# Optimization experiments

Measured on AMD Instinct MI355X. Metric: run time of the kernel, lower is better.

The kernel has to match this reference:

```python
import jax, jax.numpy as jnp
import numpy as np

B, S, D, H = 2, 2048, 1024, 16
HD = D // H


def setup_inputs() -> dict:
    key = jax.random.key(0)
    ks = jax.random.split(key, 5)
    x = jax.random.normal(ks[0], (B, S, D), dtype=jnp.float32)
    qk_w = jax.random.normal(ks[1], (D, 2 * D), dtype=jnp.float32) * 0.02
    qk_b = jnp.zeros((2 * D,), dtype=jnp.float32)
    v_w = jax.random.normal(ks[2], (D, D), dtype=jnp.float32) * 0.02
    cproj_w = jax.random.normal(ks[3], (D, D), dtype=jnp.float32) * 0.02
    resid_gain = jnp.ones((1, H, 1, 1), dtype=jnp.float32)
    skip_gain = jnp.ones((1, H, 1, 1), dtype=jnp.float32)
    centre_gain = jnp.ones((1, H, 1, 1), dtype=jnp.float32)
    return {"x": x, "qk_w": qk_w, "qk_b": qk_b, "v_w": v_w,
            "cproj_w": cproj_w, "resid_gain": resid_gain,
            "skip_gain": skip_gain, "centre_gain": centre_gain}


def reference(x, qk_w, qk_b, v_w, cproj_w, resid_gain, skip_gain, centre_gain):
    b, s, d = x.shape
    h, hd = H, d // H
    # fused QK projection (pconv with bias)
    qk = x @ qk_w + qk_b                      # [B,S,2D]
    q, k = jnp.split(qk, 2, axis=-1)
    v = x @ v_w                               # [B,S,D] (pconv, bias=0)
    # split heads -> [B,H,S,hd]
    q = q.reshape(b, s, h, hd).transpose(0, 2, 1, 3)
    k = k.reshape(b, s, h, hd).transpose(0, 2, 1, 3)
    v = v.reshape(b, s, h, hd).transpose(0, 2, 1, 3)
    # scaled QK^T with causal mask
    scores = jnp.einsum('bhqd,bhkd->bhqk', q, k) / jnp.sqrt(jnp.float32(hd))
    causal = jnp.tril(jnp.ones((s, s), dtype=bool))
    neg = jnp.finfo(scores.dtype).min
    scores = jnp.where(causal, scores, neg)
    attn = jax.nn.softmax(scores, axis=-1)    # [B,H,S,S]
    # shaped attention: per-head resid gain + skip (identity) - centred uniform causal
    row = jnp.arange(1, s + 1, dtype=jnp.float32)
    uniform = jnp.tril(jnp.ones((s, s), dtype=jnp.float32) / row[:, None])  # [S,S]
    eye = jnp.eye(s, dtype=jnp.float32)
    new_attn = (resid_gain * attn
                + skip_gain * eye[None, None]
                - centre_gain * uniform[None, None])
    out = jnp.einsum('bhqk,bhkd->bhqd', new_attn, v)  # [B,H,S,hd]
    out = out.transpose(0, 2, 1, 3).reshape(b, s, d)  # merge heads
    out = out @ cproj_w                                # c_proj (bias=0)
    return out
```

## Files before the change

### kernel.cpp

```cpp
#include <hip/hip_runtime.h>
#include <hip/hip_bf16.h>


typedef __hip_bfloat16 bf16;
typedef short s16x8 __attribute__((ext_vector_type(8)));
typedef short s16x4 __attribute__((ext_vector_type(4)));
typedef float f32x4 __attribute__((ext_vector_type(4)));

#define NB 2
#define NS 2048
#define ND 1024
#define NH 16
#define NHD 64
#define QSCALE 0.18033688011112042f
#define SW(r) (((r) & 7) << 4)

__device__ __forceinline__ float b2f(unsigned short u) {
  union { float f; unsigned int i; } c; c.i = ((unsigned int)u) << 16; return c.f;
}

__device__ __forceinline__ unsigned short f2bu(float f) {
  bf16 t = __float2bfloat16(f);
  unsigned short u;
  __builtin_memcpy(&u, &t, 2);
  return u;
}

__device__ __forceinline__ void gload_lds16(const void* g, void* l) {
  __builtin_amdgcn_global_load_lds((const __attribute__((address_space(1))) void*)g,
                                   (__attribute__((address_space(3))) void*)l, 16, 0, 0);
}

__global__ __launch_bounds__(256) void prologue(const float* __restrict__ x,
                                                const float* __restrict__ qk_w,
                                                const float* __restrict__ v_w,
                                                const float* __restrict__ cp_w,
                                                bf16* __restrict__ xb,
                                                bf16* __restrict__ qkwt,
                                                bf16* __restrict__ vwt,
                                                bf16* __restrict__ cpwt) {
  const int z = blockIdx.z;
  const int tx = threadIdx.x, ty = threadIdx.y;
  if (z == 0) {
    const int lb = (int)blockIdx.x + 64 * (int)blockIdx.y;
    const int base = lb * 2048 + (ty * 32 + tx) * 8;
    float4 v0 = *(const float4*)(x + base);
    float4 v1 = *(const float4*)(x + base + 4);
    ushort4 o0, o1;
    o0.x = f2bu(v0.x); o0.y = f2bu(v0.y); o0.z = f2bu(v0.z); o0.w = f2bu(v0.w);
    o1.x = f2bu(v1.x); o1.y = f2bu(v1.y); o1.z = f2bu(v1.z); o1.w = f2bu(v1.w);
    *(ushort4*)(xb + base) = o0;
    *(ushort4*)(xb + base + 4) = o1;
    return;
  }
  const int N = (z == 1) ? 2048 : 1024;
  if ((int)blockIdx.x * 32 >= N) return;
  const float* in = (z == 1) ? qk_w : (z == 2) ? v_w : cp_w;
  bf16* out = (z == 1) ? qkwt : (z == 2) ? vwt : cpwt;
  const int K = 1024;
  __shared__ float tile[32][33];
  int nt = blockIdx.x * 32, kt = blockIdx.y * 32;
#pragma unroll
  for (int j = 0; j < 32; j += 8)
    tile[ty + j][tx] = in[(size_t)(kt + ty + j) * N + nt + tx];
  __syncthreads();
#pragma unroll
  for (int j = 0; j < 32; j += 8)
    out[(size_t)(nt + ty + j) * K + kt + tx] = __float2bfloat16(tile[tx][ty + j]);
}

__global__ __launch_bounds__(256) void gemm_qkv(const bf16* __restrict__ A,
                                                const bf16* __restrict__ BtQK,
                                                const bf16* __restrict__ BtV,
                                                const float* __restrict__ bias,
                                                bf16* __restrict__ qo, bf16* __restrict__ ko,
                                                bf16* __restrict__ vo) {
  __shared__ alignas(16) bf16 As[128 * 32];
  __shared__ alignas(16) bf16 Bs[128 * 32];
  const int K = 1024;
  const int tid = threadIdx.x;
  const int wave = tid >> 6, lane = tid & 63;
  const int l15 = lane & 15, lg = lane >> 4;
  const int wr = wave >> 1, wc = wave & 1;
  const int bid = (int)blockIdx.x + (int)blockIdx.y * 24;
  const int sbid = (bid & 7) * 96 + (bid >> 3);
  const int brow = (sbid / 24) * 128, bcol = (sbid % 24) * 128;
  const bf16* Bsrc = (bcol < 2048) ? (BtQK + (size_t)bcol * K)
                                   : (BtV + (size_t)(bcol - 2048) * K);

  f32x4 acc[4][4] = {};
  const int r0 = tid >> 2;
  const int kc = (tid & 3) * 8;
  char* AsB = (char*)As;
  char* BsB = (char*)Bs;

  for (int k0 = 0; k0 < K; k0 += 32) {
    gload_lds16(A + (size_t)(brow + r0) * K + k0 + kc, AsB + tid * 16);
    gload_lds16(A + (size_t)(brow + r0 + 64) * K + k0 + kc, AsB + 4096 + tid * 16);
    gload_lds16(Bsrc + (size_t)r0 * K + k0 + kc, BsB + tid * 16);
    gload_lds16(Bsrc + (size_t)(r0 + 64) * K + k0 + kc, BsB + 4096 + tid * 16);
    __syncthreads();
    s16x8 af[4], bfr[4];
#pragma unroll
    for (int mi = 0; mi < 4; ++mi)
      af[mi] = *(const s16x8*)(As + (wr * 64 + mi * 16 + l15) * 32 + lg * 8);
#pragma unroll
    for (int ni = 0; ni < 4; ++ni)
      bfr[ni] = *(const s16x8*)(Bs + (wc * 64 + ni * 16 + l15) * 32 + lg * 8);
#pragma unroll
    for (int mi = 0; mi < 4; ++mi)
#pragma unroll
      for (int ni = 0; ni < 4; ++ni)
        acc[mi][ni] = __builtin_amdgcn_mfma_f32_16x16x32_bf16(af[mi], bfr[ni], acc[mi][ni], 0, 0, 0);
    __syncthreads();
  }

#pragma unroll
  for (int mi = 0; mi < 4; ++mi)
#pragma unroll
    for (int ni = 0; ni < 4; ++ni)
#pragma unroll
      for (int r = 0; r < 4; ++r) {
        int row = brow + wr * 64 + mi * 16 + lg * 4 + r;
        int col = bcol + wc * 64 + ni * 16 + l15;
        float v = acc[mi][ni][r];
        int b = row >> 11, s = row & 2047;
        int cc = col & 1023;
        int h = cc >> 6, e = cc & 63;
        if (col < 1024) {
          v = (v + bias[col]) * QSCALE;
          qo[((((size_t)b * NH + h) * NS) + s) * NHD + e] = __float2bfloat16(v);
        } else if (col < 2048) {
          v += bias[col];
          ko[((((size_t)b * NH + h) * NS) + s) * NHD + e] = __float2bfloat16(v);
        } else {
          vo[((((size_t)b * NH + h) * NHD) + e) * NS + s] = __float2bfloat16(v);
        }
      }
}

__global__ __launch_bounds__(256) void gemm_out(const bf16* __restrict__ A,
                                                const bf16* __restrict__ Bt,
                                                float* __restrict__ of) {
  __shared__ alignas(16) bf16 As[128 * 32];
  __shared__ alignas(16) bf16 Bs[64 * 32];
  const int K = 1024, N = 1024;
  const int tid = threadIdx.x;
  const int wave = tid >> 6, lane = tid & 63;
  const int l15 = lane & 15, lg = lane >> 4;
  const int bid = (int)blockIdx.x + (int)blockIdx.y * 16;
  const int sbid = (bid & 7) * 64 + (bid >> 3);
  const int brow = (sbid / 16) * 128, bcol = (sbid % 16) * 64;

  f32x4 acc[2][4] = {};
  const int r0 = tid >> 2;
  const int kc = (tid & 3) * 8;
  char* AsB = (char*)As;
  char* BsB = (char*)Bs;

  for (int k0 = 0; k0 < K; k0 += 32) {
    gload_lds16(A + (size_t)(brow + r0) * K + k0 + kc, AsB + tid * 16);
    gload_lds16(A + (size_t)(brow + r0 + 64) * K + k0 + kc, AsB + 4096 + tid * 16);
    gload_lds16(Bt + (size_t)(bcol + r0) * K + k0 + kc, BsB + tid * 16);
    __syncthreads();
    s16x8 af[2], bfr[4];
#pragma unroll
    for (int mi = 0; mi < 2; ++mi)
      af[mi] = *(const s16x8*)(As + (wave * 32 + mi * 16 + l15) * 32 + lg * 8);
#pragma unroll
    for (int ni = 0; ni < 4; ++ni)
      bfr[ni] = *(const s16x8*)(Bs + (ni * 16 + l15) * 32 + lg * 8);
#pragma unroll
    for (int mi = 0; mi < 2; ++mi)
#pragma unroll
      for (int ni = 0; ni < 4; ++ni)
        acc[mi][ni] = __builtin_amdgcn_mfma_f32_16x16x32_bf16(af[mi], bfr[ni], acc[mi][ni], 0, 0, 0);
    __syncthreads();
  }

#pragma unroll
  for (int mi = 0; mi < 2; ++mi)
#pragma unroll
    for (int ni = 0; ni < 4; ++ni)
#pragma unroll
      for (int r = 0; r < 4; ++r) {
        int row = brow + wave * 32 + mi * 16 + lg * 4 + r;
        int col = bcol + ni * 16 + l15;
        of[(size_t)row * N + col] = acc[mi][ni][r];
      }
}

__global__ __launch_bounds__(512, 4) void attn_kernel(const bf16* __restrict__ qb,
                                                      const bf16* __restrict__ kb,
                                                      const bf16* __restrict__ vtb,
                                                      const float* __restrict__ rg,
                                                      const float* __restrict__ sg,
                                                      const float* __restrict__ cg,
                                                      bf16* __restrict__ out) {
  const int hb = blockIdx.x;
  const int h = hb & 15, b = hb >> 4;
  const int j = blockIdx.y;
  const int tid = threadIdx.x, wave = tid >> 6, lane = tid & 63;
  const int l15 = lane & 15, lg = lane >> 4;
  const int grp = wave >> 2, wv4 = wave & 3;
  const int qt = grp ? (31 - j) : j;
  const int ntm1 = 31 - j;

  __shared__ alignas(16) char Ks[2][64 * 128];
  __shared__ alignas(16) char Vs[2][64 * 128];
  __shared__ alignas(16) char Pl[8][2048];
  char* Plw = Pl[wave];
  const int swz = ((((l15 >> 3) ^ l15) & 7) << 4);

  const size_t hoff = ((size_t)b * NH + h) * NS * NHD;
  const bf16* K = kb + hoff;
  const bf16* VT = vtb + hoff;
  const float rgh = rg[h], sgh = sg[h], cgh = cg[h];

  const int qbase = qt * 64 + wv4 * 16;
  const int qloc = wv4 * 16 + l15;

  const bf16* Q = qb + hoff;
  s16x8 qa0 = *(const s16x8*)(Q + (size_t)(qbase + l15) * NHD + lg * 8);
  s16x8 qa1 = *(const s16x8*)(Q + (size_t)(qbase + l15) * NHD + 32 + lg * 8);

  const short ONE = 0x3F80;
  const s16x8 ones = {ONE, ONE, ONE, ONE, ONE, ONE, ONE, ONE};
  s16x8 pc0, pc1;
#pragma unroll
  for (int jj = 0; jj < 8; ++jj) {
    pc0[jj] = (lg * 8 + jj <= qloc) ? ONE : (short)0;
    pc1[jj] = (32 + lg * 8 + jj <= qloc) ? ONE : (short)0;
  }

  f32x4 acc_o[4] = {};
  f32x4 acc_c[4] = {};
  f32x4 acc_l = {};

  const int srow = tid >> 3;
  const int sce = (tid & 7) * 8;
  const int scb = (sce * 2) ^ SW(srow);

  s16x8 kra = *(const s16x8*)(K + (size_t)srow * NHD + sce);
  s16x8 vra = *(const s16x8*)(VT + (size_t)srow * NS + sce);

  for (int t = 0; t <= ntm1; ++t) {
    char* Kb = Ks[t & 1];
    char* Vb = Vs[t & 1];
    *(s16x8*)(Kb + srow * 128 + scb) = kra;
    *(s16x8*)(Vb + srow * 128 + scb) = vra;
    if (t < ntm1) {
      kra = *(const s16x8*)(K + ((size_t)(t + 1) * 64 + srow) * NHD + sce);
      vra = *(const s16x8*)(VT + (size_t)srow * NS + (t + 1) * 64 + sce);
    }
    __syncthreads();

    if (t > qt) continue;
    const bool diag = (t == qt);

    f32x4 sc[4] = {};
    __builtin_amdgcn_s_setprio(1);
#pragma unroll
    for (int c = 0; c < 4; ++c) {
      const int R = c * 16 + l15;
      s16x8 kf0 = *(const s16x8*)(Kb + R * 128 + ((lg * 16) ^ SW(R)));
      s16x8 kf1 = *(const s16x8*)(Kb + R * 128 + ((64 + lg * 16) ^ SW(R)));
      sc[c] = __builtin_amdgcn_mfma_f32_16x16x32_bf16(kf0, qa0, sc[c], 0, 0, 0);
      sc[c] = __builtin_amdgcn_mfma_f32_16x16x32_bf16(kf1, qa1, sc[c], 0, 0, 0);
    }
    __builtin_amdgcn_s_setprio(0);

    if (diag) {
#pragma unroll
      for (int c = 0; c < 4; ++c)
#pragma unroll
        for (int r = 0; r < 4; ++r)
          if (c * 16 + lg * 4 + r > qloc) sc[c][r] = -INFINITY;
    }

#pragma unroll
    for (int c = 0; c < 4; ++c) {
      s16x4 pk;
      pk[0] = (short)f2bu(exp2f(sc[c][0]));
      pk[1] = (short)f2bu(exp2f(sc[c][1]));
      pk[2] = (short)f2bu(exp2f(sc[c][2]));
      pk[3] = (short)f2bu(exp2f(sc[c][3]));
      *(s16x4*)(Plw + l15 * 128 + ((c * 32 + lg * 8) ^ swz)) = pk;
    }
    s16x8 pa0 = *(const s16x8*)(Plw + l15 * 128 + ((lg * 16) ^ swz));
    s16x8 pa1 = *(const s16x8*)(Plw + l15 * 128 + ((64 + lg * 16) ^ swz));

    const s16x8 qc0 = diag ? pc0 : ones;
    const s16x8 qc1 = diag ? pc1 : ones;

    __builtin_amdgcn_s_setprio(1);
    acc_l = __builtin_amdgcn_mfma_f32_16x16x32_bf16(pa0, ones, acc_l, 0, 0, 0);
    acc_l = __builtin_amdgcn_mfma_f32_16x16x32_bf16(pa1, ones, acc_l, 0, 0, 0);
#pragma unroll
    for (int sub = 0; sub < 4; ++sub) {
      const int Rv = sub * 16 + l15;
      s16x8 vf0 = *(const s16x8*)(Vb + Rv * 128 + ((lg * 16) ^ SW(Rv)));
      s16x8 vf1 = *(const s16x8*)(Vb + Rv * 128 + ((64 + lg * 16) ^ SW(Rv)));
      acc_o[sub] = __builtin_amdgcn_mfma_f32_16x16x32_bf16(pa0, vf0, acc_o[sub], 0, 0, 0);
      acc_o[sub] = __builtin_amdgcn_mfma_f32_16x16x32_bf16(pa1, vf1, acc_o[sub], 0, 0, 0);
      acc_c[sub] = __builtin_amdgcn_mfma_f32_16x16x32_bf16(qc0, vf0, acc_c[sub], 0, 0, 0);
      acc_c[sub] = __builtin_amdgcn_mfma_f32_16x16x32_bf16(qc1, vf1, acc_c[sub], 0, 0, 0);
    }
    __builtin_amdgcn_s_setprio(0);

    if (diag) {
      float linv[4];
#pragma unroll
      for (int r = 0; r < 4; ++r) linv[r] = 1.0f / acc_l[r];
#pragma unroll
      for (int sub = 0; sub < 4; ++sub) {
        const int d = sub * 16 + l15;
        const int cb = wv4 * 32 + lg * 8;
        s16x4 vr4 = *(const s16x4*)(Vb + d * 128 + (cb ^ SW(d)));
        unsigned short vbits[4];
        __builtin_memcpy(vbits, &vr4, 8);
#pragma unroll
        for (int r = 0; r < 4; ++r) {
          int q = qbase + lg * 4 + r;
          float val = rgh * acc_o[sub][r] * linv[r] + sgh * b2f(vbits[r]) -
                      cgh * acc_c[sub][r] / (float)(q + 1);
          out[((size_t)b * NS + q) * ND + h * NHD + d] = __float2bfloat16(val);
        }
      }
    }
  }
}

extern "C" void kernel_launch(void* const* d_in, const int* in_sizes, int n_in,
                              void* d_out, int out_size, void* d_ws, size_t ws_size,
                              hipStream_t stream) {
  const float* x = (const float*)d_in[0];
  const float* qk_w = (const float*)d_in[1];
  const float* qk_b = (const float*)d_in[2];
  const float* v_w = (const float*)d_in[3];
  const float* cproj_w = (const float*)d_in[4];
  const float* rg = (const float*)d_in[5];
  const float* sg = (const float*)d_in[6];
  const float* cg = (const float*)d_in[7];
  float* out = (float*)d_out;

  char* p = (char*)d_ws;
  bf16* xb = (bf16*)p;   p += (size_t)4096 * 1024 * 2;
  bf16* qkwt = (bf16*)p; p += (size_t)2048 * 1024 * 2;
  bf16* vwt = (bf16*)p;  p += (size_t)1024 * 1024 * 2;
  bf16* cpwt = (bf16*)p; p += (size_t)1024 * 1024 * 2;
  bf16* qbuf = (bf16*)p; p += (size_t)NB * NH * NS * NHD * 2;
  bf16* kbuf = (bf16*)p; p += (size_t)NB * NH * NS * NHD * 2;
  bf16* vtbuf = (bf16*)p; p += (size_t)NB * NH * NS * NHD * 2;
  bf16* aout = (bf16*)p; p += (size_t)4096 * 1024 * 2;

  prologue<<<dim3(64, 32, 4), dim3(32, 8), 0, stream>>>(x, qk_w, v_w, cproj_w,
                                                        xb, qkwt, vwt, cpwt);
  gemm_qkv<<<dim3(24, 32), 256, 0, stream>>>(xb, qkwt, vwt, qk_b, qbuf, kbuf, vtbuf);
  attn_kernel<<<dim3(32, 16), 512, 0, stream>>>(qbuf, kbuf, vtbuf, rg, sg, cg, aout);
  gemm_out<<<dim3(16, 32), 256, 0, stream>>>(aout, cpwt, out);
}
```

Baseline: 118.7 us.

## Double-buffer LDS tiles in QKV GEMM to overlap global loads with MFMA

The QKV projection GEMM now keeps two LDS buffers for the A and B tiles. The next k-slice is prefetched with direct global-to-LDS loads while the current slice is being computed, and partial vmcnt waits replace full syncthreads. This is meant to hide global memory latency behind the MFMA work. In exchange it doubles LDS use, which can lower occupancy, and it depends on hand-written waitcnt and barrier ordering being correct.

```diff
diff --git a/kernel.cpp b/kernel.cpp
--- a/kernel.cpp
+++ b/kernel.cpp
@@ -75,8 +75,8 @@
                                                 const float* __restrict__ bias,
                                                 bf16* __restrict__ qo, bf16* __restrict__ ko,
                                                 bf16* __restrict__ vo) {
-  __shared__ alignas(16) bf16 As[128 * 32];
-  __shared__ alignas(16) bf16 Bs[128 * 32];
+  __shared__ alignas(16) bf16 As[2][128 * 32];
+  __shared__ alignas(16) bf16 Bs[2][128 * 32];
   const int K = 1024;
   const int tid = threadIdx.x;
   const int wave = tid >> 6, lane = tid & 63;
@@ -91,28 +91,49 @@
   f32x4 acc[4][4] = {};
   const int r0 = tid >> 2;
   const int kc = (tid & 3) * 8;
+  const bf16* Ag0 = A + (size_t)(brow + r0) * K + kc;
+  const bf16* Ag1 = A + (size_t)(brow + r0 + 64) * K + kc;
+  const bf16* Bg0 = Bsrc + (size_t)r0 * K + kc;
+  const bf16* Bg1 = Bsrc + (size_t)(r0 + 64) * K + kc;
   char* AsB = (char*)As;
   char* BsB = (char*)Bs;
 
-  for (int k0 = 0; k0 < K; k0 += 32) {
-    gload_lds16(A + (size_t)(brow + r0) * K + k0 + kc, AsB + tid * 16);
-    gload_lds16(A + (size_t)(brow + r0 + 64) * K + k0 + kc, AsB + 4096 + tid * 16);
-    gload_lds16(Bsrc + (size_t)r0 * K + k0 + kc, BsB + tid * 16);
-    gload_lds16(Bsrc + (size_t)(r0 + 64) * K + k0 + kc, BsB + 4096 + tid * 16);
-    __syncthreads();
+  gload_lds16(Ag0, AsB + tid * 16);
+  gload_lds16(Ag1, AsB + 4096 + tid * 16);
+  gload_lds16(Bg0, BsB + tid * 16);
+  gload_lds16(Bg1, BsB + 4096 + tid * 16);
+
+  for (int t = 0; t < 32; ++t) {
+    const int cur = t & 1;
+    if (t < 31) {
+      const int koff = (t + 1) * 32;
+      char* Aw = AsB + (cur ^ 1) * 8192;
+      char* Bw = BsB + (cur ^ 1) * 8192;
+      gload_lds16(Ag0 + koff, Aw + tid * 16);
+      gload_lds16(Ag1 + koff, Aw + 4096 + tid * 16);
+      gload_lds16(Bg0 + koff, Bw + tid * 16);
+      gload_lds16(Bg1 + koff, Bw + 4096 + tid * 16);
+      asm volatile("s_waitcnt vmcnt(4)" ::: "memory");
+    } else {
+      asm volatile("s_waitcnt vmcnt(0)" ::: "memory");
+    }
+    __builtin_amdgcn_s_barrier();
+    __builtin_amdgcn_sched_barrier(0);
+    const bf16* Ar = As[cur];
+    const bf16* Br = Bs[cur];
     s16x8 af[4], bfr[4];
 #pragma unroll
     for (int mi = 0; mi < 4; ++mi)
-      af[mi] = *(const s16x8*)(As + (wr * 64 + mi * 16 + l15) * 32 + lg * 8);
+      af[mi] = *(const s16x8*)(Ar + (wr * 64 + mi * 16 + l15) * 32 + lg * 8);
 #pragma unroll
     for (int ni = 0; ni < 4; ++ni)
-      bfr[ni] = *(const s16x8*)(Bs + (wc * 64 + ni * 16 + l15) * 32 + lg * 8);
+      bfr[ni] = *(const s16x8*)(Br + (wc * 64 + ni * 16 + l15) * 32 + lg * 8);
 #pragma unroll
     for (int mi = 0; mi < 4; ++mi)
 #pragma unroll
       for (int ni = 0; ni < 4; ++ni)
         acc[mi][ni] = __builtin_amdgcn_mfma_f32_16x16x32_bf16(af[mi], bfr[ni], acc[mi][ni], 0, 0, 0);
-    __syncthreads();
+    __builtin_amdgcn_s_barrier();
   }
 
 #pragma unroll
```

New measurement: 122.1 us (median of 2 runs). 1.03x slower.
